# Kernel tuning notes

Measured on AMD Instinct MI355X. Metric: run time of the kernel, lower is better.

## Reference

```python
import jax, jax.numpy as jnp
import numpy as np

B, C, H, W = 128, 8, 144, 144
TW, OG = 5, 2          # token_window, off_grid
NCLS, DT = 6, 256      # num_cls, dim_token
ITC = C * H * TW       # in_token_channel = 5760
EPS = 1e-5


def setup_inputs() -> dict:
    key = jax.random.key(0)
    ks = jax.random.split(key, 40)
    n = jax.random.normal
    u = jax.random.uniform
    CW = C * W  # 1152
    inp = {
        'x': n(ks[0], (B, C, H, W), jnp.float32),
        # ext head: Conv1d(1152,256,1) -> BN(256) -> Conv1d(256,2,1)
        'ext_w1': n(ks[1], (256, CW)) * 0.02, 'ext_b1': jnp.zeros((256,)),
        'ext_g': jnp.ones((256,)), 'ext_bb': jnp.zeros((256,)),
        'ext_m': n(ks[2], (256,)) * 0.1, 'ext_v': u(ks[3], (256,), minval=0.5, maxval=1.5),
        'ext_w2': n(ks[4], (2, 256)) * 0.05, 'ext_b2': jnp.zeros((2,)),
        # cls head: Conv1d(1152,256,1) -> BN(256) -> Conv1d(256,144,1)
        'cls_w1': n(ks[5], (256, CW)) * 0.02, 'cls_b1': jnp.zeros((256,)),
        'cls_g': jnp.ones((256,)), 'cls_bb': jnp.zeros((256,)),
        'cls_m': n(ks[6], (256,)) * 0.1, 'cls_v': u(ks[7], (256,), minval=0.5, maxval=1.5),
        'cls_w2': n(ks[8], (W, 256)) * 0.05, 'cls_b2': jnp.zeros((W,)),
        # to_token Linear(5760,256) and class embeddings
        'tok_w': n(ks[9], (ITC, DT)) * 0.01, 'tok_b': jnp.zeros((DT,)),
        'emb': n(ks[10], (NCLS, DT)),
        # transformer (depth=1, heads=2, dim_head=32 -> inner=64)
        'ln1_g': jnp.ones((DT,)), 'ln1_b': jnp.zeros((DT,)),
        'qkv_w': n(ks[11], (DT, 3 * 64)) * 0.05,
        'out_w': n(ks[12], (64, DT)) * 0.05, 'out_b': jnp.zeros((DT,)),
        'ln2_g': jnp.ones((DT,)), 'ln2_b': jnp.zeros((DT,)),
        'ff_w1': n(ks[13], (DT, 512)) * 0.05, 'ff_b1': jnp.zeros((512,)),
        'ff_w2': n(ks[14], (512, DT)) * 0.05, 'ff_b2': jnp.zeros((DT,)),
        'lnf_g': jnp.ones((DT,)), 'lnf_b': jnp.zeros((DT,)),
        'fin_w': n(ks[15], (DT, ITC)) * 0.02, 'fin_b': jnp.zeros((ITC,)),
    }
    return inp


def _ln(z, g, b):
    mu = jnp.mean(z, -1, keepdims=True)
    var = jnp.var(z, -1, keepdims=True)
    return (z - mu) * jax.lax.rsqrt(var + EPS) * g + b


def reference(x, ext_w1, ext_b1, ext_g, ext_bb, ext_m, ext_v, ext_w2, ext_b2,
              cls_w1, cls_b1, cls_g, cls_bb, cls_m, cls_v, cls_w2, cls_b2,
              tok_w, tok_b, emb,
              ln1_g, ln1_b, qkv_w, out_w, out_b,
              ln2_g, ln2_b, ff_w1, ff_b1, ff_w2, ff_b2,
              lnf_g, lnf_b, fin_w, fin_b):

    def head(row, w1, b1, g, bet, m, v, w2, b2):
        # row: [B, C*W, H]; 1x1 conv = per-position GEMM, BN in eval mode
        h = jnp.einsum('oc,bch->boh', w1, row) + b1[:, None]
        h = (h - m[:, None]) * jax.lax.rsqrt(v[:, None] + EPS) * g[:, None] + bet[:, None]
        h = jnp.einsum('oc,bch->boh', w2, h) + b2[:, None]
        return jnp.transpose(h, (0, 2, 1))  # [B, H, out]

    def heads_on(xx):
        # 'b c h w -> b (c w) h' (c major, w minor)
        row = jnp.transpose(xx, (0, 1, 3, 2)).reshape(B, C * W, H)
        e = jax.nn.softmax(head(row, ext_w1, ext_b1, ext_g, ext_bb, ext_m, ext_v, ext_w2, ext_b2), axis=2)
        c = jax.nn.softmax(head(row, cls_w1, cls_b1, cls_g, cls_bb, cls_m, cls_v, cls_w2, cls_b2), axis=2)
        return e, c

    ext, cls = heads_on(x)
    xp = jnp.pad(x, ((0, 0), (0, 0), (0, 0), (OG, OG)))  # [B,C,H,W+4]

    argmax_col = jnp.argmax(cls, axis=2)                  # [B,H]
    idx = argmax_col[:, :, None] + jnp.arange(TW)         # window in padded coords

    def transformer(t):  # t: [B, N, DT]
        z = _ln(t, ln1_g, ln1_b)
        q, k, v = jnp.split(z @ qkv_w, 3, axis=-1)
        sp = lambda a: a.reshape(B, -1, 2, 32).transpose(0, 2, 1, 3)  # b h n d
        q, k, v = sp(q), sp(k), sp(v)
        att = jax.nn.softmax(jnp.einsum('bhnd,bhmd->bhnm', q, k) * (32 ** -0.5), axis=-1)
        o = jnp.einsum('bhnm,bhmd->bhnd', att, v).transpose(0, 2, 1, 3).reshape(B, -1, 64)
        t = o @ out_w + out_b + t
        z = _ln(t, ln2_g, ln2_b)
        t = jax.nn.gelu(z @ ff_w1 + ff_b1, approximate=False) @ ff_w2 + ff_b2 + t
        t = _ln(t, lnf_g, lnf_b)
        return (t @ fin_w + fin_b).reshape(B, -1, C, H, TW)  # [B,N,C,H,TW]

    def refine(xpad):
        g_idx = jnp.broadcast_to(idx[:, None], (B, C, H, TW))
        patches = jnp.take_along_axis(xpad, g_idx, axis=3)    # [B,C,H,TW]
        tok = patches.reshape(B, -1) @ tok_w + tok_b          # [B,DT]
        tokens = tok[:, None, :] + emb[None]                  # [B,NCLS,DT]
        refined = transformer(tokens)                         # [B,NCLS,C,H,TW]
        xpt = jnp.transpose(xpad, (0, 2, 3, 1))               # [B,H,Wp,C]
        bb = jnp.arange(B)[:, None, None]
        hh = jnp.arange(H)[None, :, None]
        for i in range(NCLS):
            xpt = xpt.at[bb, hh, idx].set(jnp.transpose(refined[:, i], (0, 2, 3, 1)))
        return jnp.transpose(xpt, (0, 3, 1, 2))

    xp = jax.lax.cond(jnp.mean(ext[:, :, 0]) > 0.3, refine, lambda a: a, xp)
    x2 = xp[:, :, :, OG:W + OG]
    ext2, cls2 = heads_on(x2)
    return ext, cls, ext2, cls2
```

## Files before the change

### kernel.cpp

```cpp
#include <hip/hip_runtime.h>
#include <math.h>

#define EPSF 1e-5f
#define GAPTH 2e-4f
#define NKS 2
#define KSL 576
#define RROWS 18432


typedef __attribute__((ext_vector_type(8))) short short8v;
typedef __attribute__((ext_vector_type(4))) float f32x4;
typedef unsigned short ushort;
typedef unsigned int uint;

__device__ inline ushort f2bf(float f) {
    uint u = __float_as_uint(f);
    uint r = (u + 0x7FFFu + ((u >> 16) & 1u)) >> 16;
    return (ushort)r;
}
__device__ inline float bf2f(ushort h) { return __uint_as_float(((uint)h) << 16); }

__global__ __launch_bounds__(256) void wcomb_build(
    const float* __restrict__ w1e, const float* __restrict__ b1e, const float* __restrict__ ge,
    const float* __restrict__ bbe, const float* __restrict__ me, const float* __restrict__ ve,
    const float* __restrict__ w2e, const float* __restrict__ b2e,
    const float* __restrict__ w1c, const float* __restrict__ b1c, const float* __restrict__ gc,
    const float* __restrict__ bbc, const float* __restrict__ mc, const float* __restrict__ vc,
    const float* __restrict__ w2c, const float* __restrict__ b2c,
    float* __restrict__ Wc32, ushort* __restrict__ Wchi, ushort* __restrict__ Wclo,
    float* __restrict__ cconst)
{
    __shared__ float coef[256];
    __shared__ float csum[4];
    const int j = blockIdx.x, kq = blockIdx.y, tid = threadIdx.x;
    const int lane = tid & 63, wid = tid >> 6;

    const float *w1 = nullptr, *w2row = nullptr, *b1 = nullptr, *g = nullptr,
                *bb = nullptr, *m = nullptr, *v = nullptr;
    float b2v = 0.f;
    int valid = 0;
    if (j < 144) {
        valid = 1; w1 = w1c; w2row = w2c + (size_t)j * 256;
        b1 = b1c; g = gc; bb = bbc; m = mc; v = vc; b2v = b2c[j];
    } else if (j < 146) {
        valid = 1; w1 = w1e; w2row = w2e + (size_t)(j - 144) * 256;
        b1 = b1e; g = ge; bb = bbe; m = me; v = ve; b2v = b2e[j - 144];
    }

    float cf = 0.f, cc = 0.f;
    if (valid) {
        float s = g[tid] * rsqrtf(v[tid] + EPSF);
        float w2v = w2row[tid];
        cf = w2v * s;
        cc = w2v * ((b1[tid] - m[tid]) * s + bb[tid]);
    }
    coef[tid] = cf;
    if (kq == 0) {
        float t = cc;
#pragma unroll
        for (int off = 32; off; off >>= 1) t += __shfl_xor(t, off);
        if (lane == 0) csum[wid] = t;
    }
    __syncthreads();
    if (kq == 0 && tid == 0)
        cconst[j] = valid ? ((csum[0] + csum[1]) + (csum[2] + csum[3]) + b2v) : 0.f;

    for (int k = kq * 288 + tid; k < (kq + 1) * 288; k += 256) {
        float acc = 0.f;
        if (valid) {
            float a0 = 0.f, a1 = 0.f, a2 = 0.f, a3 = 0.f;
            for (int o = 0; o < 256; o += 4) {
                a0 += coef[o]     * w1[(size_t)o * 1152 + k];
                a1 += coef[o + 1] * w1[(size_t)(o + 1) * 1152 + k];
                a2 += coef[o + 2] * w1[(size_t)(o + 2) * 1152 + k];
                a3 += coef[o + 3] * w1[(size_t)(o + 3) * 1152 + k];
            }
            acc = (a0 + a1) + (a2 + a3);
        }
        Wc32[(size_t)j * 1152 + k] = acc;
        ushort hi = f2bf(acc);
        Wchi[(size_t)j * 1152 + k] = hi;
        Wclo[(size_t)j * 1152 + k] = f2bf(acc - bf2f(hi));
    }
}

__global__ void zero_counters(int* __restrict__ cand_count)
{
    *cand_count = 0;
}

__global__ __launch_bounds__(256) void transpose3(
    const float* __restrict__ s0, float* __restrict__ d0,
    const float* __restrict__ s1, float* __restrict__ d1,
    const float* __restrict__ s2, float* __restrict__ d2)
{
    const float* src; float* dst; int R, Cc;
    if (blockIdx.z == 0)      { src = s0; dst = d0; R = 256; Cc = 1152; }
    else if (blockIdx.z == 1) { src = s1; dst = d1; R = 144; Cc = 256;
                                if (blockIdx.x >= 8 || blockIdx.y >= 5) return; }
    else                      { src = s2; dst = d2; R = 160; Cc = 1152;
                                if (blockIdx.y >= 5) return; }
    __shared__ float tile[32][33];
    const int rb = blockIdx.y * 32, cb = blockIdx.x * 32;
    const int tx = threadIdx.x & 31, ty = threadIdx.x >> 5;
#pragma unroll
    for (int i = ty; i < 32; i += 8) {
        int r = rb + i, c = cb + tx;
        tile[i][tx] = (r < R && c < Cc) ? src[(size_t)r * Cc + c] : 0.f;
    }
    __syncthreads();
#pragma unroll
    for (int i = ty; i < 32; i += 8) {
        int c = cb + i, r = rb + tx;
        if (c < Cc && r < R) dst[(size_t)c * R + r] = tile[tx][i];
    }
}

__global__ __launch_bounds__(256) void logits_gemm(
    const float* __restrict__ x, const ushort* __restrict__ Wchi, const ushort* __restrict__ Wclo,
    float* __restrict__ logits_part)
{
    __shared__ ushort Ahi[64][40], Alo[64][40], Bhi[160][40], Blo[160][40];
    const int tid = threadIdx.x;
    const int lane = tid & 63, wid = tid >> 6;
    const int wm = wid & 1, wn = wid >> 1;
    const int rb = blockIdx.x * 64;
    const int ks = blockIdx.y;
    const int kbase = ks * KSL;
    const int NIT = KSL / 32;

    const int rl = tid >> 2, kk = (tid & 3) << 3;
    const int arow = rb + rl;
    const int ab = arow / 144, ahh = arow - ab * 144;

    const int br0 = tid >> 2, bk0 = (tid & 3) << 3;
    const int br2 = 128 + (tid >> 2), bk2 = (tid & 3) << 3;

    float av[8];
    short8v vbh0, vbl0, vbh1, vbl1, vbh2, vbl2;

    auto LOAD = [&](int kb) {
        int k1 = kb + kk, c1 = k1 / 144, w1 = k1 - c1 * 144;
        const float4 t0 = *reinterpret_cast<const float4*>(
            x + (((size_t)(ab * 8 + c1) * 144 + ahh) * 144 + w1));
        const float4 t1 = *reinterpret_cast<const float4*>(
            x + (((size_t)(ab * 8 + c1) * 144 + ahh) * 144 + w1 + 4));
        av[0] = t0.x; av[1] = t0.y; av[2] = t0.z; av[3] = t0.w;
        av[4] = t1.x; av[5] = t1.y; av[6] = t1.z; av[7] = t1.w;
        size_t o0 = (size_t)br0 * 1152 + kb + bk0;
        vbh0 = *reinterpret_cast<const short8v*>(Wchi + o0);
        vbl0 = *reinterpret_cast<const short8v*>(Wclo + o0);
        size_t o1 = (size_t)(br0 + 64) * 1152 + kb + bk0;
        vbh1 = *reinterpret_cast<const short8v*>(Wchi + o1);
        vbl1 = *reinterpret_cast<const short8v*>(Wclo + o1);
        if (tid < 128) {
            size_t o2 = (size_t)br2 * 1152 + kb + bk2;
            vbh2 = *reinterpret_cast<const short8v*>(Wchi + o2);
            vbl2 = *reinterpret_cast<const short8v*>(Wclo + o2);
        }
    };

    auto STORE = [&]() {
        short8v hv, lv;
#pragma unroll
        for (int q = 0; q < 8; q++) {
            ushort h = f2bf(av[q]);
            hv[q] = (short)h;
            lv[q] = (short)f2bf(av[q] - bf2f(h));
        }
        *reinterpret_cast<short8v*>(&Ahi[rl][kk]) = hv;
        *reinterpret_cast<short8v*>(&Alo[rl][kk]) = lv;
        *reinterpret_cast<short8v*>(&Bhi[br0][bk0]) = vbh0;
        *reinterpret_cast<short8v*>(&Blo[br0][bk0]) = vbl0;
        *reinterpret_cast<short8v*>(&Bhi[br0 + 64][bk0]) = vbh1;
        *reinterpret_cast<short8v*>(&Blo[br0 + 64][bk0]) = vbl1;
        if (tid < 128) {
            *reinterpret_cast<short8v*>(&Bhi[br2][bk2]) = vbh2;
            *reinterpret_cast<short8v*>(&Blo[br2][bk2]) = vbl2;
        }
    };

    f32x4 acc[2][5];
#pragma unroll
    for (int mt = 0; mt < 2; mt++)
#pragma unroll
        for (int nt = 0; nt < 5; nt++) acc[mt][nt] = (f32x4){0.f, 0.f, 0.f, 0.f};

    const int fr = lane & 15, fg = (lane >> 4) << 3;

    LOAD(kbase);
    for (int t = 0; t < NIT; t++) {
        STORE();
        if (t < NIT - 1) LOAD(kbase + (t + 1) * 32);
        __syncthreads();
        short8v ah0 = *reinterpret_cast<const short8v*>(&Ahi[wm * 32 + fr][fg]);
        short8v al0 = *reinterpret_cast<const short8v*>(&Alo[wm * 32 + fr][fg]);
        short8v ah1 = *reinterpret_cast<const short8v*>(&Ahi[wm * 32 + 16 + fr][fg]);
        short8v al1 = *reinterpret_cast<const short8v*>(&Alo[wm * 32 + 16 + fr][fg]);
#pragma unroll
        for (int nt = 0; nt < 5; nt++) {
            short8v bh = *reinterpret_cast<const short8v*>(&Bhi[wn * 80 + nt * 16 + fr][fg]);
            short8v bl = *reinterpret_cast<const short8v*>(&Blo[wn * 80 + nt * 16 + fr][fg]);
            acc[0][nt] = __builtin_amdgcn_mfma_f32_16x16x32_bf16(ah0, bh, acc[0][nt], 0, 0, 0);
            acc[0][nt] = __builtin_amdgcn_mfma_f32_16x16x32_bf16(ah0, bl, acc[0][nt], 0, 0, 0);
            acc[0][nt] = __builtin_amdgcn_mfma_f32_16x16x32_bf16(al0, bh, acc[0][nt], 0, 0, 0);
            acc[1][nt] = __builtin_amdgcn_mfma_f32_16x16x32_bf16(ah1, bh, acc[1][nt], 0, 0, 0);
            acc[1][nt] = __builtin_amdgcn_mfma_f32_16x16x32_bf16(ah1, bl, acc[1][nt], 0, 0, 0);
            acc[1][nt] = __builtin_amdgcn_mfma_f32_16x16x32_bf16(al1, bh, acc[1][nt], 0, 0, 0);
        }
        __syncthreads();
    }

    float* base = logits_part + (size_t)ks * RROWS * 160;
#pragma unroll
    for (int mt = 0; mt < 2; mt++) {
#pragma unroll
        for (int nt = 0; nt < 5; nt++) {
            int gcol = wn * 80 + nt * 16 + fr;
            if (gcol < 146) {
                float* dst = base + (size_t)(rb + wm * 32 + mt * 16 + ((lane >> 4) << 2)) * 160 + gcol;
#pragma unroll
                for (int i = 0; i < 4; i++)
                    dst[(size_t)i * 160] = acc[mt][nt][i];
            }
        }
    }
}

template<int DELTA>
__global__ __launch_bounds__(256) void softmax_heads(
    const float* __restrict__ logits_part, const float* __restrict__ cconst,
    float* __restrict__ out_cls, float* __restrict__ out_ext,
    int* __restrict__ amax, float* __restrict__ partials,
    int* __restrict__ cand_count, int* __restrict__ cand_list,
    const float* __restrict__ x, const float* __restrict__ WcT,
    const float* __restrict__ refined5, const int* __restrict__ flag)
{
    __shared__ float ps[4];
    __shared__ float dL[4][148];
    __shared__ float dsh[4][40];
    __shared__ int   ksh[4][40];
    const int r4 = threadIdx.x >> 6, lane = threadIdx.x & 63;
    const int row = blockIdx.x * 4 + r4;

    if (DELTA) {
        const int fl = *flag;
        if (fl) {
            const int b = row / 144, hh = row - b * 144;
            const int a = amax[row];
            if (lane < 40) {
                int c = lane / 5, tw = lane - c * 5;
                int w = a - 2 + tw;
                float d = 0.f; int k = 0;
                if (w >= 0 && w < 144) {
                    k = c * 144 + w;
                    d = refined5[(size_t)b * 5760 + (c * 144 + hh) * 5 + tw]
                      - x[((size_t)(b * 8 + c) * 144 + hh) * 144 + w];
                }
                dsh[r4][lane] = d; ksh[r4][lane] = k;
            }
            __syncthreads();
#pragma unroll
            for (int rj = 0; rj < 3; rj++) {
                int j = lane + rj * 64;
                if (j < 146) {
                    float acc = 0.f;
#pragma unroll 8
                    for (int i = 0; i < 40; i++)
                        acc += WcT[(size_t)ksh[r4][i] * 160 + j] * dsh[r4][i];
                    dL[r4][j] = acc;
                }
            }
        } else {
#pragma unroll
            for (int rj = 0; rj < 3; rj++) {
                int j = lane + rj * 64;
                if (j < 146) dL[r4][j] = 0.f;
            }
        }
        __syncthreads();
    }

    const float* L0 = logits_part + (size_t)row * 160;
    const float* L1 = L0 + (size_t)RROWS * 160;
    float v0 = L0[lane] + L1[lane] + cconst[lane];
    float v1 = L0[lane + 64] + L1[lane + 64] + cconst[lane + 64];
    float v2 = (lane < 16) ? (L0[lane + 128] + L1[lane + 128] + cconst[lane + 128])
                           : -3.0e38f;
    if (DELTA) {
        v0 += dL[r4][lane];
        v1 += dL[r4][lane + 64];
        if (lane < 16) v2 += dL[r4][lane + 128];
    }
    float m = v0; int mi = lane;
    if (v1 > m) { m = v1; mi = lane + 64; }
    if (v2 > m) { m = v2; mi = lane + 128; }
    float m1 = v0, m2 = -3.0e38f;
    if (v1 > m1) { m2 = m1; m1 = v1; } else m2 = v1;
    if (v2 > m1) { m2 = m1; m1 = v2; } else m2 = fmaxf(m2, v2);
#pragma unroll
    for (int off = 32; off; off >>= 1) {
        float om = __shfl_xor(m, off);
        int   oi = __shfl_xor(mi, off);
        if (om > m || (om == m && oi < mi)) { m = om; mi = oi; }
        float om1 = __shfl_xor(m1, off);
        float om2 = __shfl_xor(m2, off);
        float nm1 = fmaxf(m1, om1);
        m2 = fmaxf(fminf(m1, om1), fmaxf(m2, om2));
        m1 = nm1;
    }
    float e0 = expf(v0 - m), e1 = expf(v1 - m);
    float e2 = (lane < 16) ? expf(v2 - m) : 0.f;
    float s = e0 + e1 + e2;
#pragma unroll
    for (int off = 32; off; off >>= 1) s += __shfl_xor(s, off);
    float inv = 1.f / s;
    float* O = out_cls + (size_t)row * 144;
    O[lane] = e0 * inv;
    O[lane + 64] = e1 * inv;
    if (lane < 16) O[lane + 128] = e2 * inv;

    float l0 = L0[144] + L1[144] + cconst[144];
    float l1 = L0[145] + L1[145] + cconst[145];
    if (DELTA) { l0 += dL[r4][144]; l1 += dL[r4][145]; }
    float mx = fmaxf(l0, l1);
    float ee0 = expf(l0 - mx), ee1 = expf(l1 - mx);
    float einv = 1.f / (ee0 + ee1);
    float p0 = ee0 * einv;
    if (lane == 0) {
        out_ext[(size_t)row * 2] = p0;
        out_ext[(size_t)row * 2 + 1] = ee1 * einv;
        if (amax != nullptr && !DELTA) {
            amax[row] = mi;
            if (m1 - m2 < GAPTH) {
                int slot = atomicAdd(cand_count, 1);
                cand_list[slot] = row;
            }
        }
    }
    if (partials != nullptr) {
        if (lane == 0) ps[r4] = p0;
        __syncthreads();
        if (threadIdx.x == 0) partials[blockIdx.x] = (ps[0] + ps[1]) + (ps[2] + ps[3]);
    }
}

__global__ __launch_bounds__(256) void reduce_flag(const float* __restrict__ partials, int n,
                                                   int* __restrict__ flag)
{
    __shared__ float sm[256];
    int tid = threadIdx.x;
    float s = 0.f;
    for (int i = tid; i < n; i += 256) s += partials[i];
    sm[tid] = s; __syncthreads();
    for (int off = 128; off; off >>= 1) {
        if (tid < off) sm[tid] += sm[tid + off];
        __syncthreads();
    }
    if (tid == 0) *flag = (sm[0] * (1.f / 18432.f) > 0.3f) ? 1 : 0;
}

__global__ __launch_bounds__(256) void fixup_list(
    const int* __restrict__ cand_count, const int* __restrict__ cand_list,
    const float* __restrict__ x,
    const float* __restrict__ w1cT, const float* __restrict__ b1c,
    const float* __restrict__ gc, const float* __restrict__ bbc,
    const float* __restrict__ mc, const float* __restrict__ vc,
    const float* __restrict__ w2cT, const float* __restrict__ b2c,
    int* __restrict__ amax)
{
    __shared__ float xrow[1152];
    __shared__ float hsh[256];
    __shared__ float Lsh[144];
    const int tid = threadIdx.x;
    const int n = *cand_count;

    for (int ci = blockIdx.x; ci < n; ci += gridDim.x) {
        const int row = cand_list[ci];
        const int b = row / 144, hh = row - b * 144;
        for (int e = tid; e < 1152; e += 256) {
            int c = e / 144, w = e - c * 144;
            xrow[e] = x[(((size_t)(b * 8 + c) * 144 + hh) * 144) + w];
        }
        __syncthreads();
        {
            float a0 = 0.f, a1 = 0.f, a2 = 0.f, a3 = 0.f;
#pragma unroll 4
            for (int k = 0; k < 1152; k += 4) {
                a0 += w1cT[(size_t)k * 256 + tid] * xrow[k];
                a1 += w1cT[(size_t)(k + 1) * 256 + tid] * xrow[k + 1];
                a2 += w1cT[(size_t)(k + 2) * 256 + tid] * xrow[k + 2];
                a3 += w1cT[(size_t)(k + 3) * 256 + tid] * xrow[k + 3];
            }
            float a = (a0 + a1) + (a2 + a3);
            float sc = gc[tid] * rsqrtf(vc[tid] + EPSF);
            hsh[tid] = (a + b1c[tid] - mc[tid]) * sc + bbc[tid];
        }
        __syncthreads();
        if (tid < 144) {
            float a0 = 0.f, a1 = 0.f, a2 = 0.f, a3 = 0.f;
#pragma unroll 4
            for (int k = 0; k < 256; k += 4) {
                a0 += w2cT[(size_t)k * 144 + tid] * hsh[k];
                a1 += w2cT[(size_t)(k + 1) * 144 + tid] * hsh[k + 1];
                a2 += w2cT[(size_t)(k + 2) * 144 + tid] * hsh[k + 2];
                a3 += w2cT[(size_t)(k + 3) * 144 + tid] * hsh[k + 3];
            }
            Lsh[tid] = (a0 + a1) + (a2 + a3) + b2c[tid];
        }
        __syncthreads();
        if (tid == 0) {
            int bi = 0; float bv = Lsh[0];
            for (int j = 1; j < 144; j++) if (Lsh[j] > bv) { bv = Lsh[j]; bi = j; }
            amax[row] = bi;
        }
        __syncthreads();
    }
}

__global__ __launch_bounds__(256) void tok_partial(const float* __restrict__ x,
    const int* __restrict__ amax, const float* __restrict__ tok_w, float* __restrict__ tpart)
{
    __shared__ float P[720];
    __shared__ int ash[144];
    int b = blockIdx.x, c = blockIdx.y, tid = threadIdx.x;
    if (tid < 144) ash[tid] = amax[b * 144 + tid];
    __syncthreads();
    for (int e = tid; e < 720; e += 256) {
        int hh = e / 5, tw = e - hh * 5;
        int w = ash[hh] + tw - 2;
        P[e] = (w >= 0 && w < 144) ? x[(((size_t)(b * 8 + c) * 144 + hh) * 144) + w] : 0.f;
    }
    __syncthreads();
    const float* wbase = tok_w + (size_t)c * 720 * 256;
    float a0 = 0.f, a1 = 0.f, a2 = 0.f, a3 = 0.f;
    for (int k = 0; k < 720; k += 4) {
        a0 += P[k]     * wbase[(size_t)k * 256 + tid];
        a1 += P[k + 1] * wbase[(size_t)(k + 1) * 256 + tid];
        a2 += P[k + 2] * wbase[(size_t)(k + 2) * 256 + tid];
        a3 += P[k + 3] * wbase[(size_t)(k + 3) * 256 + tid];
    }
    tpart[((size_t)b * 8 + c) * 256 + tid] = (a0 + a1) + (a2 + a3);
}

__global__ __launch_bounds__(512) void attn_ff(
    const float* __restrict__ tpart, const float* __restrict__ tok_b,
    const float* __restrict__ emb,
    const float* __restrict__ ln1_g, const float* __restrict__ ln1_b,
    const float* __restrict__ qkv_w,
    const float* __restrict__ out_w, const float* __restrict__ out_b,
    const float* __restrict__ ln2_g, const float* __restrict__ ln2_b,
    const float* __restrict__ ff_w1, const float* __restrict__ ff_b1,
    const float* __restrict__ ff_w2, const float* __restrict__ ff_b2,
    const float* __restrict__ lnf_g, const float* __restrict__ lnf_b,
    float* __restrict__ tfin)
{
    __shared__ float s[256];
    __shared__ float z[6][256];
    __shared__ float qk[6][192];
    __shared__ float att[2][6];
    __shared__ float o5[64];
    __shared__ float t5[256];
    __shared__ float zsh[256];
    __shared__ float fsh[512];
    __shared__ float stat[2];
    const int b = blockIdx.x, tid = threadIdx.x;
    const int lane = tid & 63, wv = tid >> 6;
    const int g4 = tid >> 2, l4 = tid & 3;

    if (tid < 256) {
        float a = tok_b[tid];
#pragma unroll
        for (int ks = 0; ks < 8; ks++) a += tpart[((size_t)b * 8 + ks) * 256 + tid];
        s[tid] = a;
    }
    __syncthreads();

    if (wv < 6) {
        float y[4], s1 = 0.f, s2 = 0.f;
#pragma unroll
        for (int q = 0; q < 4; q++) {
            int k = lane + 64 * q;
            y[q] = s[k] + emb[wv * 256 + k];
            s1 += y[q]; s2 += y[q] * y[q];
        }
#pragma unroll
        for (int off = 32; off; off >>= 1) { s1 += __shfl_xor(s1, off); s2 += __shfl_xor(s2, off); }
        float mu = s1 * (1.f / 256.f);
        float var = s2 * (1.f / 256.f) - mu * mu;
        float rs = rsqrtf(var + EPSF);
#pragma unroll
        for (int q = 0; q < 4; q++) {
            int k = lane + 64 * q;
            z[wv][k] = (y[q] - mu) * rs * ln1_g[k] + ln1_b[k];
        }
    }
    __syncthreads();

    for (int tt = g4; tt < 832; tt += 128) {
        int i, c;
        if (tt < 768) { i = tt >> 7; c = 64 + (tt & 127); }
        else          { i = 5;       c = tt - 768; }
        float a = 0.f;
#pragma unroll 8
        for (int j = 0; j < 64; j++) {
            int k = l4 + 4 * j;
            a += z[i][k] * qkv_w[(size_t)k * 192 + c];
        }
        a += __shfl_xor(a, 1);
        a += __shfl_xor(a, 2);
        if (l4 == 0) qk[i][c] = a;
    }
    __syncthreads();

    if (tid < 12) {
        int h = tid / 6, j = tid - h * 6;
        float a = 0.f;
#pragma unroll
        for (int d = 0; d < 32; d++) a += qk[5][h * 32 + d] * qk[j][64 + h * 32 + d];
        att[h][j] = a * 0.17677669529663687f;
    }
    __syncthreads();
    if (tid < 2) {
        float m = -3.0e38f;
        for (int j = 0; j < 6; j++) m = fmaxf(m, att[tid][j]);
        float ssum = 0.f;
        for (int j = 0; j < 6; j++) { float e = expf(att[tid][j] - m); att[tid][j] = e; ssum += e; }
        float inv = 1.f / ssum;
        for (int j = 0; j < 6; j++) att[tid][j] *= inv;
    }
    __syncthreads();
    if (tid < 64) {
        int h = tid >> 5;
        float a = 0.f;
#pragma unroll
        for (int j = 0; j < 6; j++) a += att[h][j] * qk[j][128 + tid];
        o5[tid] = a;
    }
    __syncthreads();

    for (int tt = g4; tt < 256; tt += 128) {
        float a = 0.f;
#pragma unroll
        for (int j = 0; j < 16; j++) {
            int d = l4 + 4 * j;
            a += o5[d] * out_w[(size_t)d * 256 + tt];
        }
        a += __shfl_xor(a, 1);
        a += __shfl_xor(a, 2);
        if (l4 == 0) t5[tt] = a + out_b[tt] + s[tt] + emb[5 * 256 + tt];
    }
    __syncthreads();

    if (wv == 0) {
        float s1 = 0.f, s2 = 0.f;
#pragma unroll
        for (int q = 0; q < 4; q++) { float vv = t5[lane + 64 * q]; s1 += vv; s2 += vv * vv; }
#pragma unroll
        for (int off = 32; off; off >>= 1) { s1 += __shfl_xor(s1, off); s2 += __shfl_xor(s2, off); }
        if (lane == 0) {
            float mu = s1 * (1.f / 256.f);
            float var = s2 * (1.f / 256.f) - mu * mu;
            stat[0] = mu; stat[1] = rsqrtf(var + EPSF);
        }
    }
    __syncthreads();
    if (tid < 256)
        zsh[tid] = (t5[tid] - stat[0]) * stat[1] * ln2_g[tid] + ln2_b[tid];
    __syncthreads();

    for (int tt = g4; tt < 512; tt += 128) {
        float a = 0.f;
#pragma unroll 8
        for (int j = 0; j < 64; j++) {
            int k = l4 + 4 * j;
            a += zsh[k] * ff_w1[(size_t)k * 512 + tt];
        }
        a += __shfl_xor(a, 1);
        a += __shfl_xor(a, 2);
        if (l4 == 0) {
            a += ff_b1[tt];
            fsh[tt] = 0.5f * a * (1.f + erff(a * 0.70710678118654752f));
        }
    }
    __syncthreads();

    for (int tt = g4; tt < 256; tt += 128) {
        float a = 0.f;
#pragma unroll 8
        for (int j = 0; j < 128; j++) {
            int k = l4 + 4 * j;
            a += fsh[k] * ff_w2[(size_t)k * 256 + tt];
        }
        a += __shfl_xor(a, 1);
        a += __shfl_xor(a, 2);
        if (l4 == 0) s[tt] = a + ff_b2[tt] + t5[tt];
    }
    __syncthreads();

    if (wv == 0) {
        float s1 = 0.f, s2 = 0.f;
#pragma unroll
        for (int q = 0; q < 4; q++) { float vv = s[lane + 64 * q]; s1 += vv; s2 += vv * vv; }
#pragma unroll
        for (int off = 32; off; off >>= 1) { s1 += __shfl_xor(s1, off); s2 += __shfl_xor(s2, off); }
        if (lane == 0) {
            float mu = s1 * (1.f / 256.f);
            float var = s2 * (1.f / 256.f) - mu * mu;
            stat[0] = mu; stat[1] = rsqrtf(var + EPSF);
        }
    }
    __syncthreads();
    if (tid < 256)
        tfin[(size_t)b * 256 + tid] = (s[tid] - stat[0]) * stat[1] * lnf_g[tid] + lnf_b[tid];
}

__global__ __launch_bounds__(256) void fin_gemm(const float* __restrict__ tfin,
    const float* __restrict__ fin_w, const float* __restrict__ fin_b, float* __restrict__ refined5)
{
    __shared__ float tf[16][256];
    int tid = threadIdx.x;
    int nb = blockIdx.x * 256 + tid;
    int bg = blockIdx.y * 16;
    for (int e = tid; e < 4096; e += 256) tf[e >> 8][e & 255] = tfin[(size_t)(bg + (e >> 8)) * 256 + (e & 255)];
    __syncthreads();
    if (nb < 5760) {
        float acc[16];
#pragma unroll
        for (int bb = 0; bb < 16; bb++) acc[bb] = 0.f;
        for (int k = 0; k < 256; k++) {
            float wv = fin_w[(size_t)k * 5760 + nb];
#pragma unroll
            for (int bb = 0; bb < 16; bb++) acc[bb] += tf[bb][k] * wv;
        }
        float fb = fin_b[nb];
#pragma unroll
        for (int bb = 0; bb < 16; bb++)
            refined5[(size_t)(bg + bb) * 5760 + nb] = acc[bb] + fb;
    }
}

extern "C" void kernel_launch(void* const* d_in, const int* in_sizes, int n_in,
                              void* d_out, int out_size, void* d_ws, size_t ws_size,
                              hipStream_t stream)
{
    const float* x      = (const float*)d_in[0];
    const float* ext_w1 = (const float*)d_in[1];
    const float* ext_b1 = (const float*)d_in[2];
    const float* ext_g  = (const float*)d_in[3];
    const float* ext_bb = (const float*)d_in[4];
    const float* ext_m  = (const float*)d_in[5];
    const float* ext_v  = (const float*)d_in[6];
    const float* ext_w2 = (const float*)d_in[7];
    const float* ext_b2 = (const float*)d_in[8];
    const float* cls_w1 = (const float*)d_in[9];
    const float* cls_b1 = (const float*)d_in[10];
    const float* cls_g  = (const float*)d_in[11];
    const float* cls_bb = (const float*)d_in[12];
    const float* cls_m  = (const float*)d_in[13];
    const float* cls_v  = (const float*)d_in[14];
    const float* cls_w2 = (const float*)d_in[15];
    const float* cls_b2 = (const float*)d_in[16];
    const float* tok_w  = (const float*)d_in[17];
    const float* tok_b  = (const float*)d_in[18];
    const float* emb    = (const float*)d_in[19];
    const float* ln1_g  = (const float*)d_in[20];
    const float* ln1_b  = (const float*)d_in[21];
    const float* qkv_w  = (const float*)d_in[22];
    const float* out_w  = (const float*)d_in[23];
    const float* out_b  = (const float*)d_in[24];
    const float* ln2_g  = (const float*)d_in[25];
    const float* ln2_b  = (const float*)d_in[26];
    const float* ff_w1  = (const float*)d_in[27];
    const float* ff_b1  = (const float*)d_in[28];
    const float* ff_w2  = (const float*)d_in[29];
    const float* ff_b2  = (const float*)d_in[30];
    const float* lnf_g  = (const float*)d_in[31];
    const float* lnf_b  = (const float*)d_in[32];
    const float* fin_w  = (const float*)d_in[33];
    const float* fin_b  = (const float*)d_in[34];

    float* out = (float*)d_out;
    float* ws  = (float*)d_ws;

    float*  Wc32     = ws;
    float*  cconst   = ws + 184320;
    ushort* Wchi     = (ushort*)(ws + 184480);
    ushort* Wclo     = (ushort*)(ws + 276640);
    float*  logitsP  = ws + 368800;
    float*  partials = ws + 6267040;
    float*  tfin     = ws + 6402720;
    float*  refined5 = ws + 6435488;
    float*  tpart    = ws + 7172768;
    int*    amax     = (int*)(ws + 7434912);
    int*    flag     = (int*)(ws + 7453344);
    int*    cand_cnt = (int*)(ws + 7453345);
    int*    cand_lst = (int*)(ws + 7453346);
    float*  w1cT     = ws + 7471780;
    float*  w2cT     = ws + 7766692;
    float*  WcT      = ws + 7803556;

    float* out_ext  = out;
    float* out_cls  = out + 36864;
    float* out_ext2 = out + 2691072;
    float* out_cls2 = out + 2727936;

    dim3 blk(256);

    wcomb_build<<<dim3(160, 4), blk, 0, stream>>>(
        ext_w1, ext_b1, ext_g, ext_bb, ext_m, ext_v, ext_w2, ext_b2,
        cls_w1, cls_b1, cls_g, cls_bb, cls_m, cls_v, cls_w2, cls_b2,
        Wc32, Wchi, Wclo, cconst);
    zero_counters<<<1, 1, 0, stream>>>(cand_cnt);
    transpose3<<<dim3(36, 8, 3), blk, 0, stream>>>(cls_w1, w1cT, cls_w2, w2cT, Wc32, WcT);

    logits_gemm<<<dim3(288, NKS), blk, 0, stream>>>(x, Wchi, Wclo, logitsP);
    softmax_heads<0><<<4608, blk, 0, stream>>>(logitsP, cconst, out_cls, out_ext, amax, partials,
        cand_cnt, cand_lst, nullptr, nullptr, nullptr, nullptr);
    reduce_flag<<<1, blk, 0, stream>>>(partials, 4608, flag);
    fixup_list<<<256, blk, 0, stream>>>(cand_cnt, cand_lst, x,
        w1cT, cls_b1, cls_g, cls_bb, cls_m, cls_v, w2cT, cls_b2, amax);

    tok_partial<<<dim3(128, 8), blk, 0, stream>>>(x, amax, tok_w, tpart);
    attn_ff<<<128, dim3(512), 0, stream>>>(tpart, tok_b, emb, ln1_g, ln1_b, qkv_w,
        out_w, out_b, ln2_g, ln2_b, ff_w1, ff_b1, ff_w2, ff_b2, lnf_g, lnf_b, tfin);
    fin_gemm<<<dim3(23, 8), blk, 0, stream>>>(tfin, fin_w, fin_b, refined5);

    softmax_heads<1><<<4608, blk, 0, stream>>>(logitsP, cconst, out_cls2, out_ext2, amax, nullptr,
        nullptr, nullptr, x, WcT, refined5, flag);
}
```

Baseline: 277.0 us.

## Split fused transformer kernel into six smaller kernels for wider parallelism

Replaces the single 128-block attn_ff kernel, which ran one batch per block, with six kernels: LN1 prep, QKV GEMM over 7 blocks per batch, attention plus out-projection and LN2, FF1 split four ways, FF2 split two ways, and the final LN. The goal is to spread the small GEMV work across more workgroups and CUs than one block per batch allows. In exchange it adds five extra kernel launches and round-trips for the intermediates through global memory.

```diff
diff --git a/kernel.cpp b/kernel.cpp
--- a/kernel.cpp
+++ b/kernel.cpp
@@ -443,74 +443,93 @@
     tpart[((size_t)b * 8 + c) * 256 + tid] = (a0 + a1) + (a2 + a3);
 }
 
-__global__ __launch_bounds__(512) void attn_ff(
+__global__ __launch_bounds__(256) void prep_z(
     const float* __restrict__ tpart, const float* __restrict__ tok_b,
     const float* __restrict__ emb,
     const float* __restrict__ ln1_g, const float* __restrict__ ln1_b,
-    const float* __restrict__ qkv_w,
+    float* __restrict__ zall, float* __restrict__ sbuf)
+{
+    __shared__ float s[256];
+    __shared__ float r8[8];
+    const int b = blockIdx.x, tid = threadIdx.x;
+    const int lane = tid & 63, wv = tid >> 6;
+    float a = tok_b[tid];
+#pragma unroll
+    for (int ks = 0; ks < 8; ks++) a += tpart[((size_t)b * 8 + ks) * 256 + tid];
+    s[tid] = a;
+    sbuf[(size_t)b * 256 + tid] = a;
+    __syncthreads();
+    for (int i = 0; i < 6; i++) {
+        float v = s[tid] + emb[i * 256 + tid];
+        float s1 = v, s2 = v * v;
+#pragma unroll
+        for (int off = 32; off; off >>= 1) { s1 += __shfl_down(s1, off); s2 += __shfl_down(s2, off); }
+        if (lane == 0) { r8[wv * 2] = s1; r8[wv * 2 + 1] = s2; }
+        __syncthreads();
+        float t1 = (r8[0] + r8[2]) + (r8[4] + r8[6]);
+        float t2 = (r8[1] + r8[3]) + (r8[5] + r8[7]);
+        float mu = t1 * (1.f / 256.f);
+        float var = t2 * (1.f / 256.f) - mu * mu;
+        zall[((size_t)b * 6 + i) * 256 + tid] = (v - mu) * rsqrtf(var + EPSF) * ln1_g[tid] + ln1_b[tid];
+        __syncthreads();
+    }
+}
+
+__global__ __launch_bounds__(256) void qkv_gemm(
+    const float* __restrict__ zall, const float* __restrict__ qkv_w,
+    float* __restrict__ qkbuf)
+{
+    __shared__ float zrow[256];
+    const int b = blockIdx.x, y = blockIdx.y, tid = threadIdx.x;
+    const int i = (y < 6) ? y : 5;
+    const int g4 = tid >> 2, l4 = tid & 3;
+    zrow[tid] = zall[((size_t)b * 6 + i) * 256 + tid];
+    __syncthreads();
+    if (y < 6) {
+        for (int tt = g4; tt < 128; tt += 64) {
+            const int c = 64 + tt;
+            float a = 0.f;
+#pragma unroll 8
+            for (int j = 0; j < 64; j++) {
+                int k = l4 + 4 * j;
+                a += zrow[k] * qkv_w[(size_t)k * 192 + c];
+            }
+            a += __shfl_xor(a, 1);
+            a += __shfl_xor(a, 2);
+            if (l4 == 0) qkbuf[((size_t)b * 6 + i) * 192 + c] = a;
+        }
+    } else {
+        const int c = g4;
+        float a = 0.f;
+#pragma unroll 8
+        for (int j = 0; j < 64; j++) {
+            int k = l4 + 4 * j;
+            a += zrow[k] * qkv_w[(size_t)k * 192 + c];
+        }
+        a += __shfl_xor(a, 1);
+        a += __shfl_xor(a, 2);
+        if (l4 == 0) qkbuf[((size_t)b * 6 + 5) * 192 + c] = a;
+    }
+}
+
+__global__ __launch_bounds__(256) void attn_out(
+    const float* __restrict__ qkbuf, const float* __restrict__ sbuf,
+    const float* __restrict__ emb,
     const float* __restrict__ out_w, const float* __restrict__ out_b,
     const float* __restrict__ ln2_g, const float* __restrict__ ln2_b,
-    const float* __restrict__ ff_w1, const float* __restrict__ ff_b1,
-    const float* __restrict__ ff_w2, const float* __restrict__ ff_b2,
-    const float* __restrict__ lnf_g, const float* __restrict__ lnf_b,
-    float* __restrict__ tfin)
-{
-    __shared__ float s[256];
-    __shared__ float z[6][256];
+    float* __restrict__ z2_5, float* __restrict__ t5buf)
+{
     __shared__ float qk[6][192];
     __shared__ float att[2][6];
     __shared__ float o5[64];
     __shared__ float t5[256];
-    __shared__ float zsh[256];
-    __shared__ float fsh[512];
     __shared__ float stat[2];
     const int b = blockIdx.x, tid = threadIdx.x;
     const int lane = tid & 63, wv = tid >> 6;
     const int g4 = tid >> 2, l4 = tid & 3;
 
-    if (tid < 256) {
-        float a = tok_b[tid];
-#pragma unroll
-        for (int ks = 0; ks < 8; ks++) a += tpart[((size_t)b * 8 + ks) * 256 + tid];
-        s[tid] = a;
-    }
-    __syncthreads();
-
-    if (wv < 6) {
-        float y[4], s1 = 0.f, s2 = 0.f;
-#pragma unroll
-        for (int q = 0; q < 4; q++) {
-            int k = lane + 64 * q;
-            y[q] = s[k] + emb[wv * 256 + k];
-            s1 += y[q]; s2 += y[q] * y[q];
-        }
-#pragma unroll
-        for (int off = 32; off; off >>= 1) { s1 += __shfl_xor(s1, off); s2 += __shfl_xor(s2, off); }
-        float mu = s1 * (1.f / 256.f);
-        float var = s2 * (1.f / 256.f) - mu * mu;
-        float rs = rsqrtf(var + EPSF);
-#pragma unroll
-        for (int q = 0; q < 4; q++) {
-            int k = lane + 64 * q;
-            z[wv][k] = (y[q] - mu) * rs * ln1_g[k] + ln1_b[k];
-        }
-    }
-    __syncthreads();
-
-    for (int tt = g4; tt < 832; tt += 128) {
-        int i, c;
-        if (tt < 768) { i = tt >> 7; c = 64 + (tt & 127); }
-        else          { i = 5;       c = tt - 768; }
-        float a = 0.f;
-#pragma unroll 8
-        for (int j = 0; j < 64; j++) {
-            int k = l4 + 4 * j;
-            a += z[i][k] * qkv_w[(size_t)k * 192 + c];
-        }
-        a += __shfl_xor(a, 1);
-        a += __shfl_xor(a, 2);
-        if (l4 == 0) qk[i][c] = a;
-    }
+    for (int e = tid; e < 1152; e += 256)
+        qk[e / 192][e - (e / 192) * 192] = qkbuf[(size_t)b * 1152 + e];
     __syncthreads();
 
     if (tid < 12) {
@@ -539,7 +558,7 @@
     }
     __syncthreads();
 
-    for (int tt = g4; tt < 256; tt += 128) {
+    for (int tt = g4; tt < 256; tt += 64) {
         float a = 0.f;
 #pragma unroll
         for (int j = 0; j < 16; j++) {
@@ -548,7 +567,8 @@
         }
         a += __shfl_xor(a, 1);
         a += __shfl_xor(a, 2);
-        if (l4 == 0) t5[tt] = a + out_b[tt] + s[tt] + emb[5 * 256 + tt];
+        if (l4 == 0)
+            t5[tt] = a + out_b[tt] + sbuf[(size_t)b * 256 + tt] + emb[5 * 256 + tt];
     }
     __syncthreads();
 
@@ -565,43 +585,76 @@
         }
     }
     __syncthreads();
-    if (tid < 256)
-        zsh[tid] = (t5[tid] - stat[0]) * stat[1] * ln2_g[tid] + ln2_b[tid];
-    __syncthreads();
-
-    for (int tt = g4; tt < 512; tt += 128) {
+    t5buf[(size_t)b * 256 + tid] = t5[tid];
+    z2_5[(size_t)b * 256 + tid] = (t5[tid] - stat[0]) * stat[1] * ln2_g[tid] + ln2_b[tid];
+}
+
+__global__ __launch_bounds__(256) void ff1_gelu(
+    const float* __restrict__ z2_5, const float* __restrict__ ff_w1,
+    const float* __restrict__ ff_b1, float* __restrict__ f5)
+{
+    __shared__ float zsh[256];
+    const int b = blockIdx.x, q = blockIdx.y, tid = threadIdx.x;
+    const int g4 = tid >> 2, l4 = tid & 3;
+    zsh[tid] = z2_5[(size_t)b * 256 + tid];
+    __syncthreads();
+    for (int tt = g4; tt < 128; tt += 64) {
+        const int jj = q * 128 + tt;
         float a = 0.f;
 #pragma unroll 8
         for (int j = 0; j < 64; j++) {
             int k = l4 + 4 * j;
-            a += zsh[k] * ff_w1[(size_t)k * 512 + tt];
+            a += zsh[k] * ff_w1[(size_t)k * 512 + jj];
         }
         a += __shfl_xor(a, 1);
         a += __shfl_xor(a, 2);
         if (l4 == 0) {
-            a += ff_b1[tt];
-            fsh[tt] = 0.5f * a * (1.f + erff(a * 0.70710678118654752f));
-        }
-    }
-    __syncthreads();
-
-    for (int tt = g4; tt < 256; tt += 128) {
+            a += ff_b1[jj];
+            f5[(size_t)b * 512 + jj] = 0.5f * a * (1.f + erff(a * 0.70710678118654752f));
+        }
+    }
+}
+
+__global__ __launch_bounds__(256) void ff2_half(
+    const float* __restrict__ f5, const float* __restrict__ ff_w2,
+    const float* __restrict__ ff_b2, const float* __restrict__ t5buf,
+    float* __restrict__ t6)
+{
+    __shared__ float fsh[512];
+    const int b = blockIdx.x, h = blockIdx.y, tid = threadIdx.x;
+    const int g4 = tid >> 2, l4 = tid & 3;
+    fsh[tid] = f5[(size_t)b * 512 + tid];
+    fsh[tid + 256] = f5[(size_t)b * 512 + tid + 256];
+    __syncthreads();
+    for (int tt = g4; tt < 128; tt += 64) {
+        const int o = h * 128 + tt;
         float a = 0.f;
 #pragma unroll 8
         for (int j = 0; j < 128; j++) {
             int k = l4 + 4 * j;
-            a += fsh[k] * ff_w2[(size_t)k * 256 + tt];
+            a += fsh[k] * ff_w2[(size_t)k * 256 + o];
         }
         a += __shfl_xor(a, 1);
         a += __shfl_xor(a, 2);
-        if (l4 == 0) s[tt] = a + ff_b2[tt] + t5[tt];
-    }
-    __syncthreads();
-
+        if (l4 == 0)
+            t6[(size_t)b * 256 + o] = a + ff_b2[o] + t5buf[(size_t)b * 256 + o];
+    }
+}
+
+__global__ __launch_bounds__(256) void lnf_k(
+    const float* __restrict__ t6, const float* __restrict__ lnf_g,
+    const float* __restrict__ lnf_b, float* __restrict__ tfin)
+{
+    __shared__ float tsh[256];
+    __shared__ float stat[2];
+    const int b = blockIdx.x, tid = threadIdx.x;
+    const int lane = tid & 63, wv = tid >> 6;
+    tsh[tid] = t6[(size_t)b * 256 + tid];
+    __syncthreads();
     if (wv == 0) {
         float s1 = 0.f, s2 = 0.f;
 #pragma unroll
-        for (int q = 0; q < 4; q++) { float vv = s[lane + 64 * q]; s1 += vv; s2 += vv * vv; }
+        for (int q = 0; q < 4; q++) { float vv = tsh[lane + 64 * q]; s1 += vv; s2 += vv * vv; }
 #pragma unroll
         for (int off = 32; off; off >>= 1) { s1 += __shfl_xor(s1, off); s2 += __shfl_xor(s2, off); }
         if (lane == 0) {
@@ -611,8 +664,7 @@
         }
     }
     __syncthreads();
-    if (tid < 256)
-        tfin[(size_t)b * 256 + tid] = (s[tid] - stat[0]) * stat[1] * lnf_g[tid] + lnf_b[tid];
+    tfin[(size_t)b * 256 + tid] = (tsh[tid] - stat[0]) * stat[1] * lnf_g[tid] + lnf_b[tid];
 }
 
 __global__ __launch_bounds__(256) void fin_gemm(const float* __restrict__ tfin,
@@ -699,6 +751,13 @@
     float*  w1cT     = ws + 7471780;
     float*  w2cT     = ws + 7766692;
     float*  WcT      = ws + 7803556;
+    float*  zall     = ws + 7987876;
+    float*  sbuf     = ws + 8184484;
+    float*  qkbuf    = ws + 8217252;
+    float*  z2_5     = ws + 8364708;
+    float*  t5buf    = ws + 8397476;
+    float*  f5buf    = ws + 8430244;
+    float*  t6buf    = ws + 8495780;
 
     float* out_ext  = out;
     float* out_cls  = out + 36864;
@@ -722,8 +781,12 @@
         w1cT, cls_b1, cls_g, cls_bb, cls_m, cls_v, w2cT, cls_b2, amax);
 
     tok_partial<<<dim3(128, 8), blk, 0, stream>>>(x, amax, tok_w, tpart);
-    attn_ff<<<128, dim3(512), 0, stream>>>(tpart, tok_b, emb, ln1_g, ln1_b, qkv_w,
-        out_w, out_b, ln2_g, ln2_b, ff_w1, ff_b1, ff_w2, ff_b2, lnf_g, lnf_b, tfin);
+    prep_z<<<128, blk, 0, stream>>>(tpart, tok_b, emb, ln1_g, ln1_b, zall, sbuf);
+    qkv_gemm<<<dim3(128, 7), blk, 0, stream>>>(zall, qkv_w, qkbuf);
+    attn_out<<<128, blk, 0, stream>>>(qkbuf, sbuf, emb, out_w, out_b, ln2_g, ln2_b, z2_5, t5buf);
+    ff1_gelu<<<dim3(128, 4), blk, 0, stream>>>(z2_5, ff_w1, ff_b1, f5buf);
+    ff2_half<<<dim3(128, 2), blk, 0, stream>>>(f5buf, ff_w2, ff_b2, t5buf, t6buf);
+    lnf_k<<<128, blk, 0, stream>>>(t6buf, lnf_g, lnf_b, tfin);
     fin_gemm<<<dim3(23, 8), blk, 0, stream>>>(tfin, fin_w, fin_b, refined5);
 
     softmax_heads<1><<<4608, blk, 0, stream>>>(logitsP, cconst, out_cls2, out_ext2, amax, nullptr,
```

After: 271.3 us. 2.0% less time.
